# Kernel tuning notes

Hardware: AMD Instinct MI355X
Metric: run time of the kernel (lower is better)

The kernel has to match this reference:

```python
import jax, jax.numpy as jnp
import numpy as np

IN_DIM = 1024
OUT_DIM = 1024


def setup_inputs() -> dict:
    key = jax.random.key(0)
    k1, k2, k3, k4 = jax.random.split(key, 4)
    B, T = 4, 2048
    x = jax.random.normal(k1, (B, T, IN_DIM), dtype=jnp.float32)
    # torch Linear stores weight as [out, in]; y = x @ W.T
    s = 1.0 / np.sqrt(IN_DIM)
    Wq = jax.random.uniform(k2, (OUT_DIM, IN_DIM), jnp.float32, -s, s)
    Wk = jax.random.uniform(k3, (OUT_DIM, IN_DIM), jnp.float32, -s, s)
    Wv = jax.random.uniform(k4, (OUT_DIM, IN_DIM), jnp.float32, -s, s)
    return {"x": x, "Wq": Wq, "Wk": Wk, "Wv": Wv}


def reference(x, Wq, Wk, Wv):
    # x: [B, T, D_in]
    q = jnp.einsum('btd,od->bto', x, Wq)   # [B, T, D_out]
    k = jnp.einsum('btd,od->bto', x, Wk)
    v = jnp.einsum('btd,od->bto', x, Wv)
    T = x.shape[1]
    scores = jnp.einsum('bqo,bko->bqk', q, k)  # [B, T, T]
    causal = jnp.tril(jnp.ones((T, T), dtype=bool))  # True = keep
    scores = jnp.where(causal, scores, -jnp.inf)
    scale = 1.0 / jnp.sqrt(jnp.asarray(k.shape[-1], scores.dtype))
    weights = jax.nn.softmax(scores * scale, axis=-1)
    # dropout_value = 0.0 -> identity
    return jnp.einsum('bqk,bko->bqo', weights, v)
```

## Files before the change

### kernel.cpp

```cpp
#include <hip/hip_runtime.h>
#include <cstdint>
#include <cstddef>

typedef __attribute__((ext_vector_type(8))) short bf16x8;
typedef __attribute__((ext_vector_type(4))) float f32x4;

#define CSCALE 0.045084220027780106f

__device__ __forceinline__ void gload_lds16(const void* g, void* l) {
  __builtin_amdgcn_global_load_lds(
      (const __attribute__((address_space(1))) unsigned int*)g,
      (__attribute__((address_space(3))) unsigned int*)l, 16, 0, 0);
}

__device__ __forceinline__ unsigned short f2bf(float f) {
  unsigned int u = __float_as_uint(f);
  return (unsigned short)((u + 0x7FFFu + ((u >> 16) & 1u)) >> 16);
}

__device__ __forceinline__ float bf2f(unsigned short u) {
  return __uint_as_float((unsigned int)u << 16);
}

__global__ void cvt_kernel(const float* __restrict__ in,
                           unsigned short* __restrict__ out, int n8) {
  int i = blockIdx.x * blockDim.x + threadIdx.x;
  if (i >= n8) return;
  const float4* p = (const float4*)in + (size_t)i * 2;
  float4 a = p[0], b = p[1];
  float vals[8] = {a.x, a.y, a.z, a.w, b.x, b.y, b.z, b.w};
  union { unsigned short u[8]; uint4 v; } r;
#pragma unroll
  for (int j = 0; j < 8; ++j) r.u[j] = f2bf(vals[j]);
  ((uint4*)out)[i] = r.v;
}

__global__ void cvt3_kernel(const float* __restrict__ a,
                            const float* __restrict__ b,
                            const float* __restrict__ c,
                            unsigned short* __restrict__ oa,
                            unsigned short* __restrict__ ob,
                            unsigned short* __restrict__ oc) {
  int bid = blockIdx.x;
  const float* src;
  unsigned short* dst;
  int base;
  if (bid < 512) { src = a; dst = oa; base = bid; }
  else if (bid < 1024) { src = b; dst = ob; base = bid - 512; }
  else { src = c; dst = oc; base = bid - 1024; }
  int i = base * 256 + threadIdx.x;
  const float4* p = (const float4*)src + (size_t)i * 2;
  float4 x = p[0], y = p[1];
  float vals[8] = {x.x, x.y, x.z, x.w, y.x, y.y, y.z, y.w};
  union { unsigned short u[8]; uint4 v; } r;
#pragma unroll
  for (int j = 0; j < 8; ++j) r.u[j] = f2bf(vals[j]);
  ((uint4*)dst)[i] = r.v;
}

template <int MODE>
__device__ __forceinline__ void gemm8_body(const unsigned short* __restrict__ A,
                                           const unsigned short* __restrict__ B,
                                           void* __restrict__ Cv) {
  constexpr int LDA = (MODE <= 1) ? 1024 : 2048;
  constexpr int LDB = (MODE <= 1) ? 1024 : (MODE == 2 ? 2048 : 8192);
  constexpr int LDC =
      (MODE == 0) ? 2048 : (MODE == 1 ? 8192 : (MODE == 2 ? 2048 : 1024));

  int arow, brow, nt = 16, kb = 0;
  size_t cbase;
  if constexpr (MODE == 0 || MODE == 1) {
    arow = blockIdx.x * 256;
    brow = blockIdx.y * 128;
    cbase = (size_t)arow * LDC + blockIdx.y * 128;
  } else if constexpr (MODE == 2) {
    int qt = blockIdx.x, jt = blockIdx.y, b = blockIdx.z;
    if (jt > 2 * qt + 1) return;
    arow = b * 2048 + qt * 256;
    brow = b * 2048 + jt * 128;
    cbase = (size_t)arow * LDC + jt * 128;
  } else {
    int bm = blockIdx.x;
    int b = bm >> 3, qt = 7 - (bm & 7);
    arow = b * 2048 + qt * 256;
    brow = blockIdx.y * 128;
    kb = b * 2048;
    nt = (qt + 1) * 4;
    cbase = (size_t)arow * LDC + blockIdx.y * 128;
  }

  __shared__ unsigned short As[3][256 * 64];
  __shared__ unsigned short Bs[3][128 * 64];

  const int tid = threadIdx.x;
  const int lane = tid & 63;
  const int l15 = lane & 15, g = lane >> 4;
  const int w = tid >> 6;
  const int wm = w >> 2, wn = w & 3;

  f32x4 acc[8][2] = {};

  auto stage_op = [&](int buf, int t, int op) {
    int k0 = t * 64;
    if (op < 4) {
      int chunk = op * 512 + tid;
      int row = chunk >> 3, c8 = chunk & 7;
      int ce = (c8 * 16) ^ ((row & 7) << 4);
      gload_lds16(A + (size_t)(arow + row) * LDA + k0 + (ce >> 1),
                  &As[buf][(op * 512 + (tid & ~63)) * 8]);
    } else {
      int chunk = (op - 4) * 512 + tid;
      int row = chunk >> 3, c8 = chunk & 7;
      int ce = (c8 * 16) ^ ((row & 7) << 4);
      gload_lds16(B + (size_t)(brow + row) * LDB + kb + k0 + (ce >> 1),
                  &Bs[buf][((op - 4) * 512 + (tid & ~63)) * 8]);
    }
  };

  auto lda_frag = [&](int buf, int mt, int kk) -> bf16x8 {
    int row = wm * 128 + mt * 16 + l15;
    int byte = (row * 128 + kk * 64 + g * 16) ^ ((l15 & 7) << 4);
    return *(const bf16x8*)((const char*)&As[buf][0] + byte);
  };
  auto ldb_frag = [&](int buf, int n2, int kk) -> bf16x8 {
    int row = wn * 32 + n2 * 16 + l15;
    int byte = (row * 128 + kk * 64 + g * 16) ^ ((l15 & 7) << 4);
    return *(const bf16x8*)((const char*)&Bs[buf][0] + byte);
  };

#pragma unroll
  for (int op = 0; op < 6; ++op) stage_op(0, 0, op);
#pragma unroll
  for (int op = 0; op < 6; ++op) stage_op(1, 1, op);
  asm volatile("s_waitcnt vmcnt(6)" ::: "memory");
  __builtin_amdgcn_s_barrier();

  for (int t = 0; t < nt; ++t) {
    int buf = t % 3;
    int sbuf = (t + 2) % 3;
    bool do_stage = (t + 2) < nt;
#pragma unroll
    for (int ph = 0; ph < 2; ++ph) {
      bf16x8 af[4][2], bv[2][2];
#pragma unroll
      for (int mt = 0; mt < 4; ++mt)
#pragma unroll
        for (int kk = 0; kk < 2; ++kk)
          af[mt][kk] = lda_frag(buf, ph * 4 + mt, kk);
#pragma unroll
      for (int n2 = 0; n2 < 2; ++n2)
#pragma unroll
        for (int kk = 0; kk < 2; ++kk) bv[n2][kk] = ldb_frag(buf, n2, kk);
      if (do_stage) {
        if (ph == 0) {
          stage_op(sbuf, t + 2, 0);
          stage_op(sbuf, t + 2, 1);
          stage_op(sbuf, t + 2, 4);
        } else {
          stage_op(sbuf, t + 2, 2);
          stage_op(sbuf, t + 2, 3);
          stage_op(sbuf, t + 2, 5);
        }
      }
      __builtin_amdgcn_s_barrier();
      asm volatile("s_waitcnt lgkmcnt(0)" ::: "memory");
      __builtin_amdgcn_sched_barrier(0);
      __builtin_amdgcn_s_setprio(1);
#pragma unroll
      for (int mt = 0; mt < 4; ++mt)
#pragma unroll
        for (int n2 = 0; n2 < 2; ++n2)
#pragma unroll
          for (int kk = 0; kk < 2; ++kk)
            acc[ph * 4 + mt][n2] = __builtin_amdgcn_mfma_f32_16x16x32_bf16(
                af[mt][kk], bv[n2][kk], acc[ph * 4 + mt][n2], 0, 0, 0);
      __builtin_amdgcn_s_setprio(0);
      __builtin_amdgcn_s_barrier();
    }
    if (do_stage) {
      asm volatile("s_waitcnt vmcnt(6)" ::: "memory");
    } else if (t + 1 < nt) {
      asm volatile("s_waitcnt vmcnt(0)" ::: "memory");
    }
  }

#pragma unroll
  for (int mt = 0; mt < 8; ++mt) {
#pragma unroll
    for (int r = 0; r < 4; ++r) {
      int ro = wm * 128 + mt * 16 + g * 4 + r;
      int co = wn * 32 + l15;
      if constexpr (MODE == 3) {
        float* Cp = (float*)Cv + cbase + (size_t)ro * LDC + co;
        Cp[0] = acc[mt][0][r];
        Cp[16] = acc[mt][1][r];
      } else {
        unsigned short* Cp =
            (unsigned short*)Cv + cbase + (size_t)ro * LDC + co;
        Cp[0] = f2bf(acc[mt][0][r]);
        Cp[16] = f2bf(acc[mt][1][r]);
      }
    }
  }
}

__global__ __launch_bounds__(512) void gemm_proj(
    const unsigned short* __restrict__ A, const unsigned short* __restrict__ B,
    void* __restrict__ C) { gemm8_body<0>(A, B, C); }
__global__ __launch_bounds__(512) void gemm_vt(
    const unsigned short* __restrict__ A, const unsigned short* __restrict__ B,
    void* __restrict__ C) { gemm8_body<1>(A, B, C); }
__global__ __launch_bounds__(512) void gemm_s(
    const unsigned short* __restrict__ A, const unsigned short* __restrict__ B,
    void* __restrict__ C) { gemm8_body<2>(A, B, C); }
__global__ __launch_bounds__(512) void gemm_pv(
    const unsigned short* __restrict__ A, const unsigned short* __restrict__ B,
    void* __restrict__ C) { gemm8_body<3>(A, B, C); }

__global__ __launch_bounds__(256) void softmax_kernel(
    unsigned short* __restrict__ S) {
  const int r = blockIdx.x * 4 + (threadIdx.x >> 6);
  const int lane = threadIdx.x & 63;
  const int q = r & 2047;
  unsigned short* row = S + (size_t)r * 2048;
  const int klen = q + 1;
  const int kmax = ((q >> 8) + 1) << 8;

  float v[4][8];
  float m = -__builtin_inff();
#pragma unroll
  for (int it = 0; it < 4; ++it) {
    int base = (lane + it * 64) * 8;
    if (base < klen) {
      bf16x8 u = *(const bf16x8*)(row + base);
#pragma unroll
      for (int e = 0; e < 8; ++e) {
        float f = bf2f((unsigned short)u[e]) * CSCALE;
        v[it][e] = (base + e <= q) ? f : -__builtin_inff();
        m = fmaxf(m, v[it][e]);
      }
    } else {
#pragma unroll
      for (int e = 0; e < 8; ++e) v[it][e] = -__builtin_inff();
    }
  }
#pragma unroll
  for (int s = 1; s < 64; s <<= 1) m = fmaxf(m, __shfl_xor(m, s));

  float lsum = 0.f;
#pragma unroll
  for (int it = 0; it < 4; ++it)
#pragma unroll
    for (int e = 0; e < 8; ++e) {
      float p = exp2f(v[it][e] - m);
      v[it][e] = p;
      lsum += p;
    }
#pragma unroll
  for (int s = 1; s < 64; s <<= 1) lsum += __shfl_xor(lsum, s);
  float inv = 1.0f / lsum;

#pragma unroll
  for (int it = 0; it < 4; ++it) {
    int base = (lane + it * 64) * 8;
    if (base < kmax) {
      union { unsigned short u[8]; uint4 x; } o;
#pragma unroll
      for (int e = 0; e < 8; ++e) o.u[e] = f2bf(v[it][e] * inv);
      *(uint4*)(row + base) = o.x;
    }
  }
}

extern "C" void kernel_launch(void* const* d_in, const int* in_sizes, int n_in,
                              void* d_out, int out_size, void* d_ws,
                              size_t ws_size, hipStream_t stream) {
  const float* x = (const float*)d_in[0];
  const float* Wq = (const float*)d_in[1];
  const float* Wk = (const float*)d_in[2];
  const float* Wv = (const float*)d_in[3];
  unsigned short* ws = (unsigned short*)d_ws;
  unsigned short* xb = ws;
  unsigned short* Wqk = ws + (size_t)(8u << 20);
  unsigned short* Wvb = ws + (size_t)(10u << 20);
  unsigned short* QKb = ws + (size_t)(11u << 20);
  unsigned short* Vtb = ws + (size_t)(27u << 20);
  unsigned short* Sb = ws + (size_t)(35u << 20);

  cvt_kernel<<<4096, 256, 0, stream>>>(x, xb, 1048576);
  cvt3_kernel<<<1536, 256, 0, stream>>>(Wq, Wk, Wv, Wqk,
                                        Wqk + (size_t)(1u << 20), Wvb);
  gemm_proj<<<dim3(32, 16), 512, 0, stream>>>(xb, Wqk, QKb);
  gemm_vt<<<dim3(4, 64), 512, 0, stream>>>(Wvb, xb, Vtb);
  gemm_s<<<dim3(8, 16, 4), 512, 0, stream>>>(QKb, QKb + 1024, Sb);
  softmax_kernel<<<2048, 256, 0, stream>>>(Sb);
  gemm_pv<<<dim3(32, 8), 512, 0, stream>>>(Sb, Vtb, (float*)d_out);
}
```

Baseline: 259.4 us.

## Remap GEMM grids to 1D with XCD swizzle, compact causal tiles, restage pipeline

All four GEMM launches become 1D grids with an XCD-aware block remap, so neighbouring tiles land on the same chiplet's L2. The causal score GEMM now launches only the 288 valid lower-triangular tiles, with each index decoded through a sqrt, where before it launched a full grid and returned early. The k-loop is reorganised around a single 48KB LDS slot per stage, B fragments are loaded once per k-step, and stage issue is split as 3 A loads then 1 A plus 2 B loads. Launch bounds now ask for 2 blocks per CU, which adds register pressure.

```diff
diff --git a/kernel.cpp b/kernel.cpp
--- a/kernel.cpp
+++ b/kernel.cpp
@@ -1,6 +1,7 @@
 #include <hip/hip_runtime.h>
 #include <cstdint>
 #include <cstddef>
+#include <cmath>
 
 typedef __attribute__((ext_vector_type(8))) short bf16x8;
 typedef __attribute__((ext_vector_type(4))) float f32x4;
@@ -59,129 +60,142 @@
 }
 
 template <int MODE>
-__device__ __forceinline__ void gemm8_body(const unsigned short* __restrict__ A,
-                                           const unsigned short* __restrict__ B,
-                                           void* __restrict__ Cv) {
+__device__ __forceinline__ void gemm_body(const unsigned short* __restrict__ A,
+                                          const unsigned short* __restrict__ B,
+                                          void* __restrict__ Cv) {
   constexpr int LDA = (MODE <= 1) ? 1024 : 2048;
   constexpr int LDB = (MODE <= 1) ? 1024 : (MODE == 2 ? 2048 : 8192);
   constexpr int LDC =
       (MODE == 0) ? 2048 : (MODE == 1 ? 8192 : (MODE == 2 ? 2048 : 1024));
-
-  int arow, brow, nt = 16, kb = 0;
+  constexpr int NWG = (MODE == 0) ? 512 : (MODE == 2 ? 288 : 256);
+
+  const int wg = ((int)blockIdx.x & 7) * (NWG >> 3) + ((int)blockIdx.x >> 3);
+
+  int arow, brow, NT = 16, kb = 0;
   size_t cbase;
-  if constexpr (MODE == 0 || MODE == 1) {
-    arow = blockIdx.x * 256;
-    brow = blockIdx.y * 128;
-    cbase = (size_t)arow * LDC + blockIdx.y * 128;
+  if constexpr (MODE == 0) {
+    int bm = wg & 31, bn = wg >> 5;
+    arow = bm * 256; brow = bn * 128;
+    cbase = (size_t)arow * LDC + bn * 128;
+  } else if constexpr (MODE == 1) {
+    int bm = wg & 3, bn = wg >> 2;
+    arow = bm * 256; brow = bn * 128;
+    cbase = (size_t)arow * LDC + bn * 128;
   } else if constexpr (MODE == 2) {
-    int qt = blockIdx.x, jt = blockIdx.y, b = blockIdx.z;
-    if (jt > 2 * qt + 1) return;
+    int b = wg / 72, e = wg % 72;
+    int qt = (int)((sqrtf(4.f * (float)e + 1.f) - 1.f) * 0.5f);
+    if ((qt + 1) * (qt + 2) <= e) ++qt;
+    if (qt * (qt + 1) > e) --qt;
+    int jt = e - qt * (qt + 1);
     arow = b * 2048 + qt * 256;
     brow = b * 2048 + jt * 128;
     cbase = (size_t)arow * LDC + jt * 128;
   } else {
-    int bm = blockIdx.x;
-    int b = bm >> 3, qt = 7 - (bm & 7);
+    int n = wg & 7, r = wg >> 3;
+    int b = r >> 3, qt = 7 - (r & 7);
     arow = b * 2048 + qt * 256;
-    brow = blockIdx.y * 128;
+    brow = n * 128;
     kb = b * 2048;
-    nt = (qt + 1) * 4;
-    cbase = (size_t)arow * LDC + blockIdx.y * 128;
-  }
-
-  __shared__ unsigned short As[3][256 * 64];
-  __shared__ unsigned short Bs[3][128 * 64];
-
-  const int tid = threadIdx.x;
-  const int lane = tid & 63;
+    NT = (qt + 1) * 4;
+    cbase = (size_t)arow * LDC + n * 128;
+  }
+
+  __shared__ char lds[3][49152];
+  const int tid = threadIdx.x, lane = tid & 63;
   const int l15 = lane & 15, g = lane >> 4;
-  const int w = tid >> 6;
-  const int wm = w >> 2, wn = w & 3;
+  const int w = tid >> 6, wm = w >> 2, wn = w & 3;
 
   f32x4 acc[8][2] = {};
 
-  auto stage_op = [&](int buf, int t, int op) {
-    int k0 = t * 64;
-    if (op < 4) {
-      int chunk = op * 512 + tid;
-      int row = chunk >> 3, c8 = chunk & 7;
-      int ce = (c8 * 16) ^ ((row & 7) << 4);
-      gload_lds16(A + (size_t)(arow + row) * LDA + k0 + (ce >> 1),
-                  &As[buf][(op * 512 + (tid & ~63)) * 8]);
-    } else {
-      int chunk = (op - 4) * 512 + tid;
-      int row = chunk >> 3, c8 = chunk & 7;
-      int ce = (c8 * 16) ^ ((row & 7) << 4);
-      gload_lds16(B + (size_t)(brow + row) * LDB + kb + k0 + (ce >> 1),
-                  &Bs[buf][((op - 4) * 512 + (tid & ~63)) * 8]);
-    }
+  auto stageA1 = [&](int slot, int t2, int i) {
+    int chunk = i * 512 + tid;
+    int row = chunk >> 3;
+    int c8 = (chunk & 7) ^ (row & 7);
+    gload_lds16(A + (size_t)(arow + row) * LDA + t2 * 64 + c8 * 8,
+                &lds[slot][(chunk & ~63) * 16]);
   };
-
-  auto lda_frag = [&](int buf, int mt, int kk) -> bf16x8 {
+  auto stageB1 = [&](int slot, int t2, int i) {
+    int chunk = i * 512 + tid;
+    int row = chunk >> 3;
+    int c8 = (chunk & 7) ^ (row & 7);
+    gload_lds16(B + (size_t)(brow + row) * LDB + kb + t2 * 64 + c8 * 8,
+                &lds[slot][32768 + (chunk & ~63) * 16]);
+  };
+  auto lda_frag = [&](int slot, int mt, int kk) -> bf16x8 {
     int row = wm * 128 + mt * 16 + l15;
-    int byte = (row * 128 + kk * 64 + g * 16) ^ ((l15 & 7) << 4);
-    return *(const bf16x8*)((const char*)&As[buf][0] + byte);
+    int byte = row * 128 + ((kk * 64 + g * 16) ^ ((l15 & 7) << 4));
+    return *(const bf16x8*)&lds[slot][byte];
   };
-  auto ldb_frag = [&](int buf, int n2, int kk) -> bf16x8 {
+  auto ldb_frag = [&](int slot, int n2, int kk) -> bf16x8 {
     int row = wn * 32 + n2 * 16 + l15;
-    int byte = (row * 128 + kk * 64 + g * 16) ^ ((l15 & 7) << 4);
-    return *(const bf16x8*)((const char*)&Bs[buf][0] + byte);
+    int byte = 32768 + row * 128 + ((kk * 64 + g * 16) ^ ((l15 & 7) << 4));
+    return *(const bf16x8*)&lds[slot][byte];
   };
 
 #pragma unroll
-  for (int op = 0; op < 6; ++op) stage_op(0, 0, op);
-#pragma unroll
-  for (int op = 0; op < 6; ++op) stage_op(1, 1, op);
+  for (int i = 0; i < 4; ++i) stageA1(0, 0, i);
+#pragma unroll
+  for (int i = 0; i < 2; ++i) stageB1(0, 0, i);
+#pragma unroll
+  for (int i = 0; i < 4; ++i) stageA1(1, 1, i);
+#pragma unroll
+  for (int i = 0; i < 2; ++i) stageB1(1, 1, i);
   asm volatile("s_waitcnt vmcnt(6)" ::: "memory");
   __builtin_amdgcn_s_barrier();
 
-  for (int t = 0; t < nt; ++t) {
-    int buf = t % 3;
-    int sbuf = (t + 2) % 3;
-    bool do_stage = (t + 2) < nt;
-#pragma unroll
-    for (int ph = 0; ph < 2; ++ph) {
-      bf16x8 af[4][2], bv[2][2];
-#pragma unroll
-      for (int mt = 0; mt < 4; ++mt)
+  int slot = 0;
+  for (int j = 0; j < NT; ++j) {
+    const int ss = (slot >= 1) ? slot - 1 : 2;
+    const bool st = (j + 2) < NT;
+    bf16x8 bv[2][2], af[4][2];
+#pragma unroll
+    for (int n2 = 0; n2 < 2; ++n2)
+#pragma unroll
+      for (int kk = 0; kk < 2; ++kk) bv[n2][kk] = ldb_frag(slot, n2, kk);
+#pragma unroll
+    for (int mt = 0; mt < 4; ++mt)
+#pragma unroll
+      for (int kk = 0; kk < 2; ++kk) af[mt][kk] = lda_frag(slot, mt, kk);
+    if (st) { stageA1(ss, j + 2, 0); stageA1(ss, j + 2, 1); stageA1(ss, j + 2, 2); }
+    __builtin_amdgcn_s_barrier();
+    asm volatile("s_waitcnt lgkmcnt(0)" ::: "memory");
+    __builtin_amdgcn_sched_barrier(0);
+    __builtin_amdgcn_s_setprio(1);
+#pragma unroll
+    for (int mt = 0; mt < 4; ++mt)
+#pragma unroll
+      for (int n2 = 0; n2 < 2; ++n2)
 #pragma unroll
         for (int kk = 0; kk < 2; ++kk)
-          af[mt][kk] = lda_frag(buf, ph * 4 + mt, kk);
+          acc[mt][n2] = __builtin_amdgcn_mfma_f32_16x16x32_bf16(
+              af[mt][kk], bv[n2][kk], acc[mt][n2], 0, 0, 0);
+    __builtin_amdgcn_s_setprio(0);
+    __builtin_amdgcn_s_barrier();
+#pragma unroll
+    for (int mt = 0; mt < 4; ++mt)
+#pragma unroll
+      for (int kk = 0; kk < 2; ++kk) af[mt][kk] = lda_frag(slot, 4 + mt, kk);
+    if (st) { stageA1(ss, j + 2, 3); stageB1(ss, j + 2, 0); stageB1(ss, j + 2, 1); }
+    __builtin_amdgcn_s_barrier();
+    asm volatile("s_waitcnt lgkmcnt(0)" ::: "memory");
+    __builtin_amdgcn_sched_barrier(0);
+    __builtin_amdgcn_s_setprio(1);
+#pragma unroll
+    for (int mt = 0; mt < 4; ++mt)
 #pragma unroll
       for (int n2 = 0; n2 < 2; ++n2)
 #pragma unroll
-        for (int kk = 0; kk < 2; ++kk) bv[n2][kk] = ldb_frag(buf, n2, kk);
-      if (do_stage) {
-        if (ph == 0) {
-          stage_op(sbuf, t + 2, 0);
-          stage_op(sbuf, t + 2, 1);
-          stage_op(sbuf, t + 2, 4);
-        } else {
-          stage_op(sbuf, t + 2, 2);
-          stage_op(sbuf, t + 2, 3);
-          stage_op(sbuf, t + 2, 5);
-        }
-      }
-      __builtin_amdgcn_s_barrier();
-      asm volatile("s_waitcnt lgkmcnt(0)" ::: "memory");
-      __builtin_amdgcn_sched_barrier(0);
-      __builtin_amdgcn_s_setprio(1);
-#pragma unroll
-      for (int mt = 0; mt < 4; ++mt)
-#pragma unroll
-        for (int n2 = 0; n2 < 2; ++n2)
-#pragma unroll
-          for (int kk = 0; kk < 2; ++kk)
-            acc[ph * 4 + mt][n2] = __builtin_amdgcn_mfma_f32_16x16x32_bf16(
-                af[mt][kk], bv[n2][kk], acc[ph * 4 + mt][n2], 0, 0, 0);
-      __builtin_amdgcn_s_setprio(0);
-      __builtin_amdgcn_s_barrier();
-    }
-    if (do_stage) {
+        for (int kk = 0; kk < 2; ++kk)
+          acc[4 + mt][n2] = __builtin_amdgcn_mfma_f32_16x16x32_bf16(
+              af[mt][kk], bv[n2][kk], acc[4 + mt][n2], 0, 0, 0);
+    __builtin_amdgcn_s_setprio(0);
+    if (st) {
       asm volatile("s_waitcnt vmcnt(6)" ::: "memory");
-    } else if (t + 1 < nt) {
+    } else if (j + 2 == NT) {
       asm volatile("s_waitcnt vmcnt(0)" ::: "memory");
     }
+    __builtin_amdgcn_s_barrier();
+    slot = (slot == 2) ? 0 : slot + 1;
   }
 
 #pragma unroll
@@ -195,8 +209,7 @@
         Cp[0] = acc[mt][0][r];
         Cp[16] = acc[mt][1][r];
       } else {
-        unsigned short* Cp =
-            (unsigned short*)Cv + cbase + (size_t)ro * LDC + co;
+        unsigned short* Cp = (unsigned short*)Cv + cbase + (size_t)ro * LDC + co;
         Cp[0] = f2bf(acc[mt][0][r]);
         Cp[16] = f2bf(acc[mt][1][r]);
       }
@@ -204,18 +217,18 @@
   }
 }
 
-__global__ __launch_bounds__(512) void gemm_proj(
+__global__ __launch_bounds__(512, 2) void gemm_proj(
     const unsigned short* __restrict__ A, const unsigned short* __restrict__ B,
-    void* __restrict__ C) { gemm8_body<0>(A, B, C); }
-__global__ __launch_bounds__(512) void gemm_vt(
+    void* __restrict__ C) { gemm_body<0>(A, B, C); }
+__global__ __launch_bounds__(512, 2) void gemm_vt(
     const unsigned short* __restrict__ A, const unsigned short* __restrict__ B,
-    void* __restrict__ C) { gemm8_body<1>(A, B, C); }
-__global__ __launch_bounds__(512) void gemm_s(
+    void* __restrict__ C) { gemm_body<1>(A, B, C); }
+__global__ __launch_bounds__(512, 2) void gemm_s(
     const unsigned short* __restrict__ A, const unsigned short* __restrict__ B,
-    void* __restrict__ C) { gemm8_body<2>(A, B, C); }
-__global__ __launch_bounds__(512) void gemm_pv(
+    void* __restrict__ C) { gemm_body<2>(A, B, C); }
+__global__ __launch_bounds__(512, 2) void gemm_pv(
     const unsigned short* __restrict__ A, const unsigned short* __restrict__ B,
-    void* __restrict__ C) { gemm8_body<3>(A, B, C); }
+    void* __restrict__ C) { gemm_body<3>(A, B, C); }
 
 __global__ __launch_bounds__(256) void softmax_kernel(
     unsigned short* __restrict__ S) {
@@ -290,9 +303,9 @@
   cvt_kernel<<<4096, 256, 0, stream>>>(x, xb, 1048576);
   cvt3_kernel<<<1536, 256, 0, stream>>>(Wq, Wk, Wv, Wqk,
                                         Wqk + (size_t)(1u << 20), Wvb);
-  gemm_proj<<<dim3(32, 16), 512, 0, stream>>>(xb, Wqk, QKb);
-  gemm_vt<<<dim3(4, 64), 512, 0, stream>>>(Wvb, xb, Vtb);
-  gemm_s<<<dim3(8, 16, 4), 512, 0, stream>>>(QKb, QKb + 1024, Sb);
+  gemm_proj<<<512, 512, 0, stream>>>(xb, Wqk, QKb);
+  gemm_vt<<<256, 512, 0, stream>>>(Wvb, xb, Vtb);
+  gemm_s<<<288, 512, 0, stream>>>(QKb, QKb + 1024, Sb);
   softmax_kernel<<<2048, 256, 0, stream>>>(Sb);
-  gemm_pv<<<dim3(32, 8), 512, 0, stream>>>(Sb, Vtb, (float*)d_out);
-}
+  gemm_pv<<<256, 512, 0, stream>>>(Sb, Vtb, (float*)d_out);
+}
```

Measured after the change: 249.1 us. 1.04x faster.
